# Performance work log

Measured on AMD Instinct MI355X. Metric: run time of the kernel, lower is better.

## Reference

```python
import jax, jax.numpy as jnp
import numpy as np

PATCHSIZE = 512
SLACK = 64  # max(inputsize // 8, 32)


def make_grid(H, W, patchsize, slack):
    # numpy replica of grid_for_patches (static shapes at trace time)
    step = patchsize - slack
    gy = np.minimum(np.arange(patchsize, H + step, step), H)
    gx = np.minimum(np.arange(patchsize, W + step, step), W)
    yy, xx = np.meshgrid(gy, gx, indexing='ij')
    g = np.stack([yy, xx], axis=-1)                      # (gh, gw, 2) bottom-right corners
    grid = np.concatenate([g - patchsize, g], axis=-1)   # (gh, gw, 4) = (y0, x0, y1, x1)
    return np.maximum(grid, 0)


def paste_coords(grid, H, W, slack, i):
    # numpy replica of paste_patch coordinate math; i is a Python int
    gh, gw = grid.shape[0], grid.shape[1]
    hs = slack // 2
    lh = (grid[gh - 2, gw - 2, 2:4] - grid[gh - 1, gw - 1, 0:2]) // 2
    crop_top = np.concatenate([[0], np.full(gh - 2, hs), [lh[0]]])
    crop_left = np.concatenate([[0], np.full(gw - 2, hs), [lh[1]]])
    crop_bottom = np.concatenate([np.full(gh - 1, -hs), [H]])
    crop_right = np.concatenate([np.full(gw - 1, -hs), [W]])
    d0 = np.stack(np.meshgrid(crop_top, crop_left, indexing='ij'), axis=-1)
    d1 = np.stack(np.meshgrid(crop_bottom, crop_right, indexing='ij'), axis=-1)
    d = np.concatenate([d0, d1], axis=-1)                # (gh, gw, 4)
    di = d.reshape(-1, 4)[i]
    gi = (grid + d).reshape(-1, 4)[i]
    return [int(v) for v in di], [int(v) for v in gi]


def setup_inputs() -> dict:
    key = jax.random.key(0)
    k1, k2, k3, k4 = jax.random.split(key, 4)
    H = Wd = 4096
    x_u8 = jax.random.randint(k1, (1, H, Wd, 3), 0, 256, dtype=jnp.int32)
    y = jax.random.normal(k2, (1, 1, H, Wd), dtype=jnp.float32)
    W = jax.random.normal(k3, (1, 3, 3, 3), dtype=jnp.float32) * 0.1
    b = jax.random.normal(k4, (1,), dtype=jnp.float32) * 0.1
    return {'x_u8': x_u8, 'y': y, 'W': W, 'b': b, 'i': 40}


def reference(x_u8, y, W, b, i):
    # x_u8: (B,H,W,3) int -> BCHW float in [0,1]
    x = jnp.transpose(x_u8.astype(jnp.float32) / 255.0, (0, 3, 1, 2))
    H, Wd = x.shape[2], x.shape[3]
    grid = make_grid(H, Wd, PATCHSIZE, SLACK)
    p = grid.reshape(-1, 4)[i]  # (y0, x0, y1, x1), Python ints
    xp = x[..., int(p[0]):int(p[2]), int(p[1]):int(p[3])]  # (B,3,512,512)
    # stand-in for the UNet: single 3x3 conv, 1 output channel, + sigmoid
    yp = jax.lax.conv_general_dilated(
        xp, W, window_strides=(1, 1), padding='SAME',
        dimension_numbers=('NCHW', 'OIHW', 'NCHW')) + b[None, :, None, None]
    yp = jax.nn.sigmoid(yp)
    # maybe_new_y
    y0 = y if i > 0 else jnp.zeros((x.shape[0], 1, H, Wd), jnp.float32)
    # paste_patch
    di, gi = paste_coords(grid, H, Wd, SLACK, i)
    y_out = y0.at[..., gi[0]:gi[2], gi[1]:gi[3]].set(yp[..., di[0]:di[2], di[1]:di[3]])
    return y_out
```

## Files before the change

### kernel.cpp

```cpp
#include <hip/hip_runtime.h>
#include <math.h>

#define PATCH 512
#define SLACK 64
#define STEP  (PATCH - SLACK)
#define HS    (SLACK / 2)

__global__ void copy_base_kernel(const float* __restrict__ y,
                                 float* __restrict__ out,
                                 const int* __restrict__ ip,
                                 int n4) {
    int idx = blockIdx.x * blockDim.x + threadIdx.x;
    if (idx >= n4) return;
    const int i = *ip;
    const float4* __restrict__ y4 = (const float4*)y;
    float4* __restrict__ o4 = (float4*)out;
    if (i > 0) {
        o4[idx] = y4[idx];
    } else {
        o4[idx] = make_float4(0.f, 0.f, 0.f, 0.f);
    }
}

__global__ void patch_conv_kernel(const int* __restrict__ x,
                                  const float* __restrict__ Wt,
                                  const float* __restrict__ bp,
                                  const int* __restrict__ ip,
                                  float* __restrict__ out,
                                  int H, int W) {
    const int i = *ip;

    const int gh = (H - PATCH + STEP - 1) / STEP + 1;
    const int gw = (W - PATCH + STEP - 1) / STEP + 1;
    const int r = i / gw;
    const int c = i % gw;
    const int gyr = min(PATCH + r * STEP, H);
    const int gxc = min(PATCH + c * STEP, W);
    const int p0 = max(gyr - PATCH, 0);
    const int p1 = max(gxc - PATCH, 0);

    const int gy_m2 = min(PATCH + (gh - 2) * STEP, H);
    const int gx_m2 = min(PATCH + (gw - 2) * STEP, W);
    const int gy_m1 = min(PATCH + (gh - 1) * STEP, H);
    const int gx_m1 = min(PATCH + (gw - 1) * STEP, W);
    const int lh0 = (gy_m2 - (gy_m1 - PATCH)) / 2;
    const int lh1 = (gx_m2 - (gx_m1 - PATCH)) / 2;

    const int di0 = (r == 0) ? 0 : ((r == gh - 1) ? lh0 : HS);
    const int di1 = (c == 0) ? 0 : ((c == gw - 1) ? lh1 : HS);
    const int di2 = (r < gh - 1) ? (PATCH - HS) : PATCH;
    const int di3 = (c < gw - 1) ? (PATCH - HS) : PATCH;

    const int gi0 = p0 + di0;
    const int gi1 = p1 + di1;
    const int ph = di2 - di0;
    const int pw = di3 - di1;

    const int tx = blockIdx.x * blockDim.x + threadIdx.x;
    const int ty = blockIdx.y * blockDim.y + threadIdx.y;
    if (ty >= ph || tx >= pw) return;

    const int py = di0 + ty;
    const int px = di1 + tx;

    const float bias = *bp;
    const float inv255 = 1.0f / 255.0f;

    float acc = bias;
#pragma unroll
    for (int ky = 0; ky < 3; ++ky) {
        const int ppy = py + ky - 1;
        if (ppy < 0 || ppy >= PATCH) continue;
        const int ih = p0 + ppy;
#pragma unroll
        for (int kx = 0; kx < 3; ++kx) {
            const int ppx = px + kx - 1;
            if (ppx < 0 || ppx >= PATCH) continue;
            const int iw = p1 + ppx;
            const int* __restrict__ xp = x + ((size_t)ih * W + iw) * 3;
            const float w0 = Wt[0 * 9 + ky * 3 + kx];
            const float w1 = Wt[1 * 9 + ky * 3 + kx];
            const float w2 = Wt[2 * 9 + ky * 3 + kx];
            acc += w0 * ((float)xp[0] * inv255)
                 + w1 * ((float)xp[1] * inv255)
                 + w2 * ((float)xp[2] * inv255);
        }
    }

    const float v = 1.0f / (1.0f + expf(-acc));
    out[(size_t)(gi0 + ty) * W + (gi1 + tx)] = v;
}

extern "C" void kernel_launch(void* const* d_in, const int* in_sizes, int n_in,
                              void* d_out, int out_size, void* d_ws, size_t ws_size,
                              hipStream_t stream) {
    const int*   x  = (const int*)d_in[0];
    const float* y  = (const float*)d_in[1];
    const float* Wt = (const float*)d_in[2];
    const float* b  = (const float*)d_in[3];
    const int*   ip = (const int*)d_in[4];
    float* out = (float*)d_out;

    int H = 1;
    while ((long long)(H + 1) * (H + 1) <= (long long)out_size) ++H;
    const int Wd = H;

    const int n4 = (H * Wd) / 4;
    const int threads = 256;
    const int blocks = (n4 + threads - 1) / threads;
    copy_base_kernel<<<blocks, threads, 0, stream>>>(y, out, ip, n4);

    dim3 blk(32, 8);
    dim3 grd((PATCH + blk.x - 1) / blk.x, (PATCH + blk.y - 1) / blk.y);
    patch_conv_kernel<<<grd, blk, 0, stream>>>(x, Wt, b, ip, out, H, Wd);
}
```

Measured before the change: 30.08 us.

## Fuse base copy and patch convolution into one row-tiled kernel

Result: slower. 32.17 us (+6.9%).

```diff
diff --git a/kernel.cpp b/kernel.cpp
--- a/kernel.cpp
+++ b/kernel.cpp
@@ -6,66 +6,44 @@
 #define STEP  (PATCH - SLACK)
 #define HS    (SLACK / 2)
 
-__global__ void copy_base_kernel(const float* __restrict__ y,
-                                 float* __restrict__ out,
-                                 const int* __restrict__ ip,
-                                 int n4) {
-    int idx = blockIdx.x * blockDim.x + threadIdx.x;
-    if (idx >= n4) return;
-    const int i = *ip;
-    const float4* __restrict__ y4 = (const float4*)y;
-    float4* __restrict__ o4 = (float4*)out;
-    if (i > 0) {
-        o4[idx] = y4[idx];
-    } else {
-        o4[idx] = make_float4(0.f, 0.f, 0.f, 0.f);
-    }
-}
+struct Geom {
+    int p0, p1;
+    int gi0, gi1;
+    int ph, pw;
+};
 
-__global__ void patch_conv_kernel(const int* __restrict__ x,
-                                  const float* __restrict__ Wt,
-                                  const float* __restrict__ bp,
-                                  const int* __restrict__ ip,
-                                  float* __restrict__ out,
-                                  int H, int W) {
-    const int i = *ip;
-
+__device__ __forceinline__ Geom compute_geom(int i, int H, int W) {
     const int gh = (H - PATCH + STEP - 1) / STEP + 1;
     const int gw = (W - PATCH + STEP - 1) / STEP + 1;
     const int r = i / gw;
     const int c = i % gw;
     const int gyr = min(PATCH + r * STEP, H);
     const int gxc = min(PATCH + c * STEP, W);
-    const int p0 = max(gyr - PATCH, 0);
-    const int p1 = max(gxc - PATCH, 0);
-
+    Geom g;
+    g.p0 = max(gyr - PATCH, 0);
+    g.p1 = max(gxc - PATCH, 0);
     const int gy_m2 = min(PATCH + (gh - 2) * STEP, H);
     const int gx_m2 = min(PATCH + (gw - 2) * STEP, W);
     const int gy_m1 = min(PATCH + (gh - 1) * STEP, H);
     const int gx_m1 = min(PATCH + (gw - 1) * STEP, W);
     const int lh0 = (gy_m2 - (gy_m1 - PATCH)) / 2;
     const int lh1 = (gx_m2 - (gx_m1 - PATCH)) / 2;
-
     const int di0 = (r == 0) ? 0 : ((r == gh - 1) ? lh0 : HS);
     const int di1 = (c == 0) ? 0 : ((c == gw - 1) ? lh1 : HS);
     const int di2 = (r < gh - 1) ? (PATCH - HS) : PATCH;
     const int di3 = (c < gw - 1) ? (PATCH - HS) : PATCH;
+    g.gi0 = g.p0 + di0;
+    g.gi1 = g.p1 + di1;
+    g.ph  = di2 - di0;
+    g.pw  = di3 - di1;
+    return g;
+}
 
-    const int gi0 = p0 + di0;
-    const int gi1 = p1 + di1;
-    const int ph = di2 - di0;
-    const int pw = di3 - di1;
-
-    const int tx = blockIdx.x * blockDim.x + threadIdx.x;
-    const int ty = blockIdx.y * blockDim.y + threadIdx.y;
-    if (ty >= ph || tx >= pw) return;
-
-    const int py = di0 + ty;
-    const int px = di1 + tx;
-
-    const float bias = *bp;
+__device__ __forceinline__ float conv_px(const int* __restrict__ x,
+                                         const float* __restrict__ Wt,
+                                         float bias, int py, int px,
+                                         int p0, int p1, int W) {
     const float inv255 = 1.0f / 255.0f;
-
     float acc = bias;
 #pragma unroll
     for (int ky = 0; ky < 3; ++ky) {
@@ -78,17 +56,49 @@
             if (ppx < 0 || ppx >= PATCH) continue;
             const int iw = p1 + ppx;
             const int* __restrict__ xp = x + ((size_t)ih * W + iw) * 3;
-            const float w0 = Wt[0 * 9 + ky * 3 + kx];
-            const float w1 = Wt[1 * 9 + ky * 3 + kx];
-            const float w2 = Wt[2 * 9 + ky * 3 + kx];
-            acc += w0 * ((float)xp[0] * inv255)
-                 + w1 * ((float)xp[1] * inv255)
-                 + w2 * ((float)xp[2] * inv255);
+            acc += Wt[0 * 9 + ky * 3 + kx] * ((float)xp[0] * inv255)
+                 + Wt[1 * 9 + ky * 3 + kx] * ((float)xp[1] * inv255)
+                 + Wt[2 * 9 + ky * 3 + kx] * ((float)xp[2] * inv255);
         }
     }
+    return 1.0f / (1.0f + expf(-acc));
+}
 
-    const float v = 1.0f / (1.0f + expf(-acc));
-    out[(size_t)(gi0 + ty) * W + (gi1 + tx)] = v;
+__global__ __launch_bounds__(256) void fused_kernel(
+        const int* __restrict__ x, const float* __restrict__ y,
+        const float* __restrict__ Wt, const float* __restrict__ bp,
+        const int* __restrict__ ip, float* __restrict__ out,
+        int H, int W) {
+    const int w4 = W >> 2;
+    const int row = blockIdx.y;
+    const int q = blockIdx.x * blockDim.x + threadIdx.x;
+    if (q >= w4) return;
+    const int c0 = q << 2;
+    const int i = *ip;
+    const Geom g = compute_geom(i, H, W);
+
+    const size_t idx = (size_t)row * w4 + q;
+    float4 v;
+    const bool rowin = (row >= g.gi0) && (row < g.gi0 + g.ph);
+    if (!rowin || (c0 + 3 < g.gi1) || (c0 >= g.gi1 + g.pw)) {
+        v = (i > 0) ? ((const float4*)y)[idx]
+                    : make_float4(0.f, 0.f, 0.f, 0.f);
+    } else {
+        const float bias = *bp;
+        float vv[4];
+#pragma unroll
+        for (int j = 0; j < 4; ++j) {
+            const int col = c0 + j;
+            if (col >= g.gi1 && col < g.gi1 + g.pw) {
+                vv[j] = conv_px(x, Wt, bias, row - g.p0, col - g.p1,
+                                g.p0, g.p1, W);
+            } else {
+                vv[j] = (i > 0) ? y[(size_t)row * W + col] : 0.f;
+            }
+        }
+        v = make_float4(vv[0], vv[1], vv[2], vv[3]);
+    }
+    ((float4*)out)[idx] = v;
 }
 
 extern "C" void kernel_launch(void* const* d_in, const int* in_sizes, int n_in,
@@ -105,12 +115,8 @@
     while ((long long)(H + 1) * (H + 1) <= (long long)out_size) ++H;
     const int Wd = H;
 
-    const int n4 = (H * Wd) / 4;
-    const int threads = 256;
-    const int blocks = (n4 + threads - 1) / threads;
-    copy_base_kernel<<<blocks, threads, 0, stream>>>(y, out, ip, n4);
-
-    dim3 blk(32, 8);
-    dim3 grd((PATCH + blk.x - 1) / blk.x, (PATCH + blk.y - 1) / blk.y);
-    patch_conv_kernel<<<grd, blk, 0, stream>>>(x, Wt, b, ip, out, H, Wd);
+    const int w4 = Wd >> 2;
+    dim3 blk(256, 1);
+    dim3 grd((w4 + 255) / 256, H);
+    fused_kernel<<<grd, blk, 0, stream>>>(x, y, Wt, b, ip, out, H, Wd);
 }
```
